# Kernel optimization log

Measured on AMD Instinct MI355X. Metric: run time of the kernel, lower is better.

## Reference

```python
import jax, jax.numpy as jnp
import numpy as np

B, T, D_IN, D_MODEL = 4, 4096, 256, 128


def setup_inputs() -> dict:
    key = jax.random.key(0)
    ks = jax.random.split(key, 7)
    s_in = 1.0 / np.sqrt(D_IN)
    return {
        "x": jax.random.normal(ks[0], (B, T, D_IN), dtype=jnp.float32),
        "Wq": jax.random.normal(ks[1], (D_IN, D_MODEL), dtype=jnp.float32) * s_in,
        "bq": jnp.zeros((D_MODEL,), dtype=jnp.float32),
        "Wk": jax.random.normal(ks[2], (D_IN, D_MODEL), dtype=jnp.float32) * s_in,
        "bk": jnp.zeros((D_MODEL,), dtype=jnp.float32),
        "Wv": jax.random.normal(ks[3], (D_IN, D_MODEL), dtype=jnp.float32) * s_in,
        "bv": jnp.zeros((D_MODEL,), dtype=jnp.float32),
    }


def reference(x, Wq, bq, Wk, bk, Wv, bv):
    # projections: (B,T,d_in) @ (d_in,d_model) -> (B,T,d_model)
    q = x @ Wq + bq
    k = x @ Wk + bk
    v = x @ Wv + bv
    # scores: (B,T,T), scaled by sqrt(d_model)
    scores = jnp.einsum("btd,bsd->bts", q, k) / np.sqrt(D_MODEL).astype(np.float32)
    attn = jax.nn.softmax(scores, axis=-1)
    out = jnp.einsum("bts,bsd->btd", attn, v)
    return out, attn
```

## Files before the change

### kernel.cpp

```cpp
#include <hip/hip_runtime.h>
#include <hip/hip_bf16.h>
#include <stdint.h>

#define TT 4096
#define DM 128
#define DIN 256
#define NB 4

typedef __attribute__((ext_vector_type(4))) float f32x4;
typedef __attribute__((ext_vector_type(8))) short s16x8;
typedef __attribute__((ext_vector_type(4))) short s16x4;
typedef __attribute__((ext_vector_type(4))) int i32x4;

union v4u { i32x4 u; s16x8 h; };

__device__ __forceinline__ unsigned short f2bf(float f) {
    union { float f; unsigned int u; } v; v.f = f;
    return (unsigned short)((v.u + 0x7FFFu + ((v.u >> 16) & 1u)) >> 16);
}

__device__ __forceinline__ void cp16(const void* g, void* l) {
    __builtin_amdgcn_global_load_lds(
        (__attribute__((address_space(1))) unsigned int*)(size_t)g,
        (__attribute__((address_space(3))) unsigned int*)l, 16, 0, 0);
}

__global__ __launch_bounds__(256) void k_wt(const float* __restrict__ Wq,
                                            const float* __restrict__ Wk,
                                            const float* __restrict__ Wv,
                                            unsigned short* __restrict__ Wtb) {
    int tid = blockIdx.x * 256 + threadIdx.x;
    int m = tid >> 15;
    int r = tid & 32767;
    int n = r >> 8;
    int k = r & 255;
    const float* W = (m == 0) ? Wq : (m == 1) ? Wk : Wv;
    Wtb[(size_t)tid] = f2bf(W[k * DM + n]);
}

__global__ __launch_bounds__(256) void k_proj(const float* __restrict__ x,
        const float* __restrict__ bq, const float* __restrict__ bk, const float* __restrict__ bv,
        const unsigned short* __restrict__ Wtb,
        unsigned short* __restrict__ Qb, unsigned short* __restrict__ Kb,
        unsigned short* __restrict__ Vb) {
    __shared__ __align__(16) unsigned short wt[DM][40];
    __shared__ __align__(16) unsigned short xl[64][40];
    int m = blockIdx.x >> 8;
    int tile = blockIdx.x & 255;
    int rowbase = tile * 64;
    int i = threadIdx.x;
    int w = i >> 6, l = i & 63;
    int lg = l >> 4, ll = l & 15;
    const float* bias = (m == 0) ? bq : (m == 1) ? bk : bv;
    unsigned short* out = (m == 0) ? Qb : (m == 1) ? Kb : Vb;
    const unsigned short* wsrc = Wtb + (size_t)m * DM * DIN;

    f32x4 acc[8];
    for (int n = 0; n < 8; n++) acc[n] = (f32x4){0.f, 0.f, 0.f, 0.f};

    for (int kk = 0; kk < 8; kk++) {
        int k0 = kk * 32;
        for (int t = 0; t < 2; t++) {
            int idx = i + t * 256;
            int row = idx >> 2, c8 = idx & 3;
            s16x8 v = *(const s16x8*)(wsrc + (size_t)row * DIN + k0 + c8 * 8);
            *(s16x8*)(&wt[row][c8 * 8]) = v;
        }
        for (int t = 0; t < 2; t++) {
            int idx = i + t * 256;
            int row = idx >> 3, c4 = idx & 7;
            f32x4 v = *(const f32x4*)(x + (size_t)(rowbase + row) * DIN + k0 + c4 * 4);
            s16x4 h;
            for (int j = 0; j < 4; j++) h[j] = (short)f2bf(v[j]);
            *(s16x4*)(&xl[row][c4 * 4]) = h;
        }
        __syncthreads();
        s16x8 a = *(const s16x8*)(&xl[w * 16 + ll][lg * 8]);
        for (int n = 0; n < 8; n++) {
            s16x8 b = *(const s16x8*)(&wt[n * 16 + ll][lg * 8]);
            acc[n] = __builtin_amdgcn_mfma_f32_16x16x32_bf16(a, b, acc[n], 0, 0, 0);
        }
        __syncthreads();
    }
    for (int n = 0; n < 8; n++) {
        int col = n * 16 + ll;
        float bv_ = bias[col];
        for (int j = 0; j < 4; j++) {
            int row = rowbase + w * 16 + lg * 4 + j;
            out[(size_t)row * DM + col] = f2bf(acc[n][j] + bv_);
        }
    }
}

__global__ __launch_bounds__(256) void k_vt(const unsigned short* __restrict__ Vb,
                                            unsigned short* __restrict__ Vtb) {
    __shared__ __align__(16) unsigned short tile[64][72];
    int bid = blockIdx.x;
    int b = bid >> 7;
    int rem = bid & 127;
    int tI = rem >> 1, dI = rem & 1;
    int t0 = tI * 64, d0 = dI * 64;
    int i = threadIdx.x;
    for (int t = 0; t < 2; t++) {
        int idx = i + t * 256;
        int r = idx >> 3, c8 = idx & 7;
        s16x8 v = *(const s16x8*)(Vb + ((size_t)(b * TT) + t0 + r) * DM + d0 + c8 * 8);
        *(s16x8*)(&tile[r][c8 * 8]) = v;
    }
    __syncthreads();
    for (int t = 0; t < 2; t++) {
        int idx = i + t * 256;
        int r2 = idx >> 3, c8 = idx & 7;
        s16x8 v;
        for (int j = 0; j < 8; j++) v[j] = (short)tile[c8 * 8 + j][r2];
        *(s16x8*)(Vtb + ((size_t)b * DM + d0 + r2) * TT + t0 + c8 * 8) = v;
    }
}

__global__ __launch_bounds__(512, 4) void k_attn(const unsigned short* __restrict__ Qb,
        const unsigned short* __restrict__ Kb, const unsigned short* __restrict__ Vtb,
        float* __restrict__ outO, float* __restrict__ outA) {
    __shared__ __align__(16) char smem[66048];

    int bid = blockIdx.x;
    int id2 = (bid & 7) * 64 + (bid >> 3);
    int b = id2 >> 7;
    int rowbase = (id2 & 127) * 32;
    int i = threadIdx.x;
    int w = i >> 6, l = i & 63;
    int rg = w & 1, ks = w >> 1;
    int lg = l >> 4, ll = l & 15;

    const unsigned short* Qrow = Qb + ((size_t)(b * TT) + rowbase) * DM;
    const unsigned short* Krow = Kb + (size_t)(b * TT) * DM;
    const unsigned short* Vt_b = Vtb + (size_t)b * DM * TT;
    const float scale = 0.08838834764831845f;

    float* rsx = (float*)(smem + 65536);

    s16x8 qf[4];
    for (int c = 0; c < 4; c++)
        qf[c] = *(const s16x8*)(Qrow + (size_t)(rg * 16 + ll) * DM + c * 32 + lg * 8);

    int kr = ks * 16 + ll;

    auto stage_k = [&](char* kbuf, int s0) {
        for (int u = 0; u < 2; u++) {
            int ch = u * 8 + w;
            int row = ch * 4 + (l >> 4);
            int g = (l & 15) ^ (row & 7);
            cp16(Krow + (size_t)(s0 + row) * DM + g * 8, kbuf + ch * 1024);
        }
    };
    auto stage_v = [&](char* vbuf, int s0) {
        for (int u = 0; u < 2; u++) {
            int ch = u * 8 + w;
            int row = ch * 8 + (l >> 3);
            int g = (l & 7) ^ (row & 7);
            cp16(Vt_b + (size_t)row * TT + s0 + g * 8, vbuf + ch * 1024);
        }
    };
    auto qk = [&](const char* kbuf) -> f32x4 {
        const char* kbase = kbuf + kr * 256;
        f32x4 acc = (f32x4){0.f, 0.f, 0.f, 0.f};
        for (int c = 0; c < 4; c++) {
            s16x8 kf = *(const s16x8*)(kbase + (((c * 4 + lg) ^ (kr & 7)) << 4));
            acc = __builtin_amdgcn_mfma_f32_16x16x32_bf16(kf, qf[c], acc, 0, 0, 0);
        }
        return acc;
    };

    float rs = 0.f;
    stage_k(smem, 0);
    stage_k(smem + 16384, 64);
    asm volatile("s_waitcnt vmcnt(2)" ::: "memory");
    __builtin_amdgcn_s_barrier();
    for (int t = 0; t < 64; t++) {
        if (t + 2 < 64) stage_k(smem + ((t + 2) & 3) * 16384, (t + 2) * 64);
        asm volatile("" ::: "memory");
        f32x4 acc = qk(smem + (t & 3) * 16384);
        for (int j = 0; j < 4; j++) rs += __expf(acc[j] * scale);
        if (t + 2 < 64) asm volatile("s_waitcnt vmcnt(2)" ::: "memory");
        else            asm volatile("s_waitcnt vmcnt(0)" ::: "memory");
        __builtin_amdgcn_s_barrier();
    }
    rs += __shfl_xor(rs, 16, 64);
    rs += __shfl_xor(rs, 32, 64);
    if (lg == 0) rsx[w * 16 + ll] = rs;
    __syncthreads();
    float inv = 1.0f / (rsx[(0 * 2 + rg) * 16 + ll] + rsx[(1 * 2 + rg) * 16 + ll]
                      + rsx[(2 * 2 + rg) * 16 + ll] + rsx[(3 * 2 + rg) * 16 + ll]);

    f32x4 oacc[8];
    for (int n = 0; n < 8; n++) oacc[n] = (f32x4){0.f, 0.f, 0.f, 0.f};

    float* Arow = outA + ((size_t)(b * TT) + rowbase + rg * 16 + ll) * TT + ks * 16 + lg * 4;
    int a0addr = (((2 * lg) & 3) * 16 + ll) * 4;
    int a1addr = (((2 * lg + 1) & 3) * 16 + ll) * 4;
    int gi = ks * 2 + (lg & 1);

    stage_k(smem, 0);
    stage_v(smem + 32768, 0);
    asm volatile("s_waitcnt vmcnt(0)" ::: "memory");
    __builtin_amdgcn_s_barrier();

    for (int t = 0; t < 64; t++) {
        size_t s0 = (size_t)t * 64;
        if (t < 63) {
            stage_k(smem + ((t + 1) & 1) * 16384, t * 64 + 64);
            stage_v(smem + 32768 + ((t + 1) & 1) * 16384, t * 64 + 64);
        }
        asm volatile("" ::: "memory");
        f32x4 acc = qk(smem + (t & 1) * 16384);
        f32x4 p;
        for (int j = 0; j < 4; j++) p[j] = __expf(acc[j] * scale) * inv;
        __builtin_nontemporal_store(p, (f32x4*)(Arow + s0));
        unsigned u0 = (unsigned)f2bf(p[0]) | ((unsigned)f2bf(p[1]) << 16);
        unsigned u1 = (unsigned)f2bf(p[2]) | ((unsigned)f2bf(p[3]) << 16);
        int b0 = __builtin_amdgcn_ds_bpermute(a0addr, (int)u0);
        int b1 = __builtin_amdgcn_ds_bpermute(a0addr, (int)u1);
        int b2 = __builtin_amdgcn_ds_bpermute(a1addr, (int)u0);
        int b3 = __builtin_amdgcn_ds_bpermute(a1addr, (int)u1);
        v4u pa;
        pa.u = (lg < 2) ? (i32x4){b0, b1, b2, b3} : (i32x4){0, 0, 0, 0};
        const char* vbuf = smem + 32768 + (t & 1) * 16384;
        for (int n = 0; n < 8; n++) {
            int vr = n * 16 + ll;
            s16x8 bfr = *(const s16x8*)(vbuf + vr * 128 + ((gi ^ (vr & 7)) << 4));
            oacc[n] = __builtin_amdgcn_mfma_f32_16x16x32_bf16(pa.h, bfr, oacc[n], 0, 0, 0);
        }
        asm volatile("s_waitcnt vmcnt(1)" ::: "memory");
        __builtin_amdgcn_s_barrier();
    }

    float* obuf = (float*)smem;
    if (ks > 0) {
        float* dst = obuf + (size_t)(rg * 3 + ks - 1) * 16 * 132;
        for (int n = 0; n < 8; n++)
            for (int j = 0; j < 4; j++)
                dst[(lg * 4 + j) * 132 + n * 16 + ll] = oacc[n][j];
    }
    __syncthreads();
    if (ks == 0) {
        float* d0 = obuf + (size_t)(rg * 3 + 0) * 16 * 132;
        float* d1 = obuf + (size_t)(rg * 3 + 1) * 16 * 132;
        float* d2 = obuf + (size_t)(rg * 3 + 2) * 16 * 132;
        for (int n = 0; n < 8; n++)
            for (int j = 0; j < 4; j++) {
                int idx = (lg * 4 + j) * 132 + n * 16 + ll;
                d0[idx] = oacc[n][j] + d0[idx] + d1[idx] + d2[idx];
            }
    }
    __syncthreads();
    {
        int row = i >> 4;
        int col = (i & 15) * 8;
        const float* src = obuf + (size_t)((row >> 4) * 3) * 16 * 132 + (row & 15) * 132 + col;
        f32x4 v0 = *(const f32x4*)(src);
        f32x4 v1 = *(const f32x4*)(src + 4);
        float* dst = outO + ((size_t)(b * TT) + rowbase + row) * DM + col;
        *(f32x4*)dst = v0;
        *(f32x4*)(dst + 4) = v1;
    }
}

extern "C" void kernel_launch(void* const* d_in, const int* in_sizes, int n_in,
                              void* d_out, int out_size, void* d_ws, size_t ws_size,
                              hipStream_t stream) {
    const float* x  = (const float*)d_in[0];
    const float* Wq = (const float*)d_in[1];
    const float* bq = (const float*)d_in[2];
    const float* Wk = (const float*)d_in[3];
    const float* bk = (const float*)d_in[4];
    const float* Wv = (const float*)d_in[5];
    const float* bv = (const float*)d_in[6];
    float* outO = (float*)d_out;
    float* outA = outO + (size_t)NB * TT * DM;

    char* ws = (char*)d_ws;
    unsigned short* Qb  = (unsigned short*)(ws);
    unsigned short* Kb  = (unsigned short*)(ws + ((size_t)1 << 22));
    unsigned short* Vb  = (unsigned short*)(ws + ((size_t)2 << 22));
    unsigned short* Vtb = (unsigned short*)(ws + ((size_t)3 << 22));
    unsigned short* Wtb = (unsigned short*)(ws + ((size_t)4 << 22));

    k_wt<<<dim3(384), dim3(256), 0, stream>>>(Wq, Wk, Wv, Wtb);
    k_proj<<<dim3(768), dim3(256), 0, stream>>>(x, bq, bk, bv, Wtb, Qb, Kb, Vb);
    k_vt<<<dim3(512), dim3(256), 0, stream>>>(Vb, Vtb);
    k_attn<<<dim3(512), dim3(512), 0, stream>>>(Qb, Kb, Vtb, outO, outA);
}
```

Before: 145.3 us.

## Warp-specialize second attention pass into producer QK waves and consumer PV waves

The second pass is split by wave. Four waves compute QK^T and the softmax probabilities for 32-column tiles and write fp32 and bf16 P tiles into shared memory. The other four waves stream V, run the PV MFMAs one tile behind, and write the attention matrix out from shared memory. Each consumer wave owns a distinct output slice, so the cross-wave reduction of O through shared memory is no longer needed. The change uses more LDS, which may reduce occupancy, and the tile-sized steps double the number of barriers.

```diff
diff --git a/kernel.cpp b/kernel.cpp
--- a/kernel.cpp
+++ b/kernel.cpp
@@ -10,9 +10,7 @@
 typedef __attribute__((ext_vector_type(4))) float f32x4;
 typedef __attribute__((ext_vector_type(8))) short s16x8;
 typedef __attribute__((ext_vector_type(4))) short s16x4;
-typedef __attribute__((ext_vector_type(4))) int i32x4;
-
-union v4u { i32x4 u; s16x8 h; };
+typedef __attribute__((ext_vector_type(2))) unsigned int u32x2;
 
 __device__ __forceinline__ unsigned short f2bf(float f) {
     union { float f; unsigned int u; } v; v.f = f;
@@ -120,7 +118,7 @@
 __global__ __launch_bounds__(512, 4) void k_attn(const unsigned short* __restrict__ Qb,
         const unsigned short* __restrict__ Kb, const unsigned short* __restrict__ Vtb,
         float* __restrict__ outO, float* __restrict__ outA) {
-    __shared__ __align__(16) char smem[66048];
+    __shared__ __align__(16) char smem[79360];
 
     int bid = blockIdx.x;
     int id2 = (bid & 7) * 64 + (bid >> 3);
@@ -128,139 +126,175 @@
     int rowbase = (id2 & 127) * 32;
     int i = threadIdx.x;
     int w = i >> 6, l = i & 63;
-    int rg = w & 1, ks = w >> 1;
     int lg = l >> 4, ll = l & 15;
+    int rh = w & 1;
 
     const unsigned short* Qrow = Qb + ((size_t)(b * TT) + rowbase) * DM;
     const unsigned short* Krow = Kb + (size_t)(b * TT) * DM;
     const unsigned short* Vt_b = Vtb + (size_t)b * DM * TT;
     const float scale = 0.08838834764831845f;
 
-    float* rsx = (float*)(smem + 65536);
+    float* rsx = (float*)(smem + 78848);
 
     s16x8 qf[4];
     for (int c = 0; c < 4; c++)
-        qf[c] = *(const s16x8*)(Qrow + (size_t)(rg * 16 + ll) * DM + c * 32 + lg * 8);
-
-    int kr = ks * 16 + ll;
-
-    auto stage_k = [&](char* kbuf, int s0) {
-        for (int u = 0; u < 2; u++) {
-            int ch = u * 8 + w;
-            int row = ch * 4 + (l >> 4);
-            int g = (l & 15) ^ (row & 7);
-            cp16(Krow + (size_t)(s0 + row) * DM + g * 8, kbuf + ch * 1024);
-        }
-    };
-    auto stage_v = [&](char* vbuf, int s0) {
-        for (int u = 0; u < 2; u++) {
-            int ch = u * 8 + w;
-            int row = ch * 8 + (l >> 3);
-            int g = (l & 7) ^ (row & 7);
-            cp16(Vt_b + (size_t)row * TT + s0 + g * 8, vbuf + ch * 1024);
-        }
-    };
-    auto qk = [&](const char* kbuf) -> f32x4 {
-        const char* kbase = kbuf + kr * 256;
-        f32x4 acc = (f32x4){0.f, 0.f, 0.f, 0.f};
-        for (int c = 0; c < 4; c++) {
-            s16x8 kf = *(const s16x8*)(kbase + (((c * 4 + lg) ^ (kr & 7)) << 4));
-            acc = __builtin_amdgcn_mfma_f32_16x16x32_bf16(kf, qf[c], acc, 0, 0, 0);
-        }
-        return acc;
-    };
+        qf[c] = *(const s16x8*)(Qrow + (size_t)(rh * 16 + ll) * DM + c * 32 + lg * 8);
 
     float rs = 0.f;
-    stage_k(smem, 0);
-    stage_k(smem + 16384, 64);
-    asm volatile("s_waitcnt vmcnt(2)" ::: "memory");
-    __builtin_amdgcn_s_barrier();
-    for (int t = 0; t < 64; t++) {
-        if (t + 2 < 64) stage_k(smem + ((t + 2) & 3) * 16384, (t + 2) * 64);
-        asm volatile("" ::: "memory");
-        f32x4 acc = qk(smem + (t & 3) * 16384);
-        for (int j = 0; j < 4; j++) rs += __expf(acc[j] * scale);
-        if (t + 2 < 64) asm volatile("s_waitcnt vmcnt(2)" ::: "memory");
-        else            asm volatile("s_waitcnt vmcnt(0)" ::: "memory");
+    {
+        int ks = w >> 1;
+        int kr = ks * 16 + ll;
+        auto stage1 = [&](int slot, int t) {
+            int s0 = t * 64;
+            for (int u = 0; u < 2; u++) {
+                int c = u * 8 + w;
+                int row = c * 4 + (l >> 4);
+                int g = (l & 15) ^ (row & 7);
+                cp16(Krow + (size_t)(s0 + row) * DM + g * 8, smem + slot * 16384 + c * 1024);
+            }
+        };
+        stage1(0, 0); stage1(1, 1);
+        asm volatile("s_waitcnt vmcnt(2)" ::: "memory");
         __builtin_amdgcn_s_barrier();
+        int cur = 0, nxt = 2;
+        for (int t = 0; t < 64; t++) {
+            if (t + 2 < 64) stage1(nxt, t + 2);
+            const char* kbase = smem + cur * 16384 + kr * 256;
+            f32x4 acc = (f32x4){0.f, 0.f, 0.f, 0.f};
+            for (int c = 0; c < 4; c++) {
+                s16x8 kf = *(const s16x8*)(kbase + (((c * 4 + lg) ^ (kr & 7)) << 4));
+                acc = __builtin_amdgcn_mfma_f32_16x16x32_bf16(kf, qf[c], acc, 0, 0, 0);
+            }
+            for (int j = 0; j < 4; j++) rs += __expf(acc[j] * scale);
+            if (t + 2 < 64) asm volatile("s_waitcnt vmcnt(2)" ::: "memory");
+            else            asm volatile("s_waitcnt vmcnt(0)" ::: "memory");
+            __builtin_amdgcn_s_barrier();
+            cur++; if (cur == 3) cur = 0;
+            nxt++; if (nxt == 3) nxt = 0;
+        }
     }
     rs += __shfl_xor(rs, 16, 64);
     rs += __shfl_xor(rs, 32, 64);
-    if (lg == 0) rsx[w * 16 + ll] = rs;
+    if (l < 16) rsx[w * 16 + l] = rs;
     __syncthreads();
-    float inv = 1.0f / (rsx[(0 * 2 + rg) * 16 + ll] + rsx[(1 * 2 + rg) * 16 + ll]
-                      + rsx[(2 * 2 + rg) * 16 + ll] + rsx[(3 * 2 + rg) * 16 + ll]);
-
-    f32x4 oacc[8];
-    for (int n = 0; n < 8; n++) oacc[n] = (f32x4){0.f, 0.f, 0.f, 0.f};
-
-    float* Arow = outA + ((size_t)(b * TT) + rowbase + rg * 16 + ll) * TT + ks * 16 + lg * 4;
-    int a0addr = (((2 * lg) & 3) * 16 + ll) * 4;
-    int a1addr = (((2 * lg + 1) & 3) * 16 + ll) * 4;
-    int gi = ks * 2 + (lg & 1);
-
-    stage_k(smem, 0);
-    stage_v(smem + 32768, 0);
-    asm volatile("s_waitcnt vmcnt(0)" ::: "memory");
-    __builtin_amdgcn_s_barrier();
-
-    for (int t = 0; t < 64; t++) {
-        size_t s0 = (size_t)t * 64;
-        if (t < 63) {
-            stage_k(smem + ((t + 1) & 1) * 16384, t * 64 + 64);
-            stage_v(smem + 32768 + ((t + 1) & 1) * 16384, t * 64 + 64);
-        }
-        asm volatile("" ::: "memory");
-        f32x4 acc = qk(smem + (t & 1) * 16384);
-        f32x4 p;
-        for (int j = 0; j < 4; j++) p[j] = __expf(acc[j] * scale) * inv;
-        __builtin_nontemporal_store(p, (f32x4*)(Arow + s0));
-        unsigned u0 = (unsigned)f2bf(p[0]) | ((unsigned)f2bf(p[1]) << 16);
-        unsigned u1 = (unsigned)f2bf(p[2]) | ((unsigned)f2bf(p[3]) << 16);
-        int b0 = __builtin_amdgcn_ds_bpermute(a0addr, (int)u0);
-        int b1 = __builtin_amdgcn_ds_bpermute(a0addr, (int)u1);
-        int b2 = __builtin_amdgcn_ds_bpermute(a1addr, (int)u0);
-        int b3 = __builtin_amdgcn_ds_bpermute(a1addr, (int)u1);
-        v4u pa;
-        pa.u = (lg < 2) ? (i32x4){b0, b1, b2, b3} : (i32x4){0, 0, 0, 0};
-        const char* vbuf = smem + 32768 + (t & 1) * 16384;
-        for (int n = 0; n < 8; n++) {
-            int vr = n * 16 + ll;
-            s16x8 bfr = *(const s16x8*)(vbuf + vr * 128 + ((gi ^ (vr & 7)) << 4));
-            oacc[n] = __builtin_amdgcn_mfma_f32_16x16x32_bf16(pa.h, bfr, oacc[n], 0, 0, 0);
-        }
-        asm volatile("s_waitcnt vmcnt(1)" ::: "memory");
-        __builtin_amdgcn_s_barrier();
-    }
-
-    float* obuf = (float*)smem;
-    if (ks > 0) {
-        float* dst = obuf + (size_t)(rg * 3 + ks - 1) * 16 * 132;
-        for (int n = 0; n < 8; n++)
-            for (int j = 0; j < 4; j++)
-                dst[(lg * 4 + j) * 132 + n * 16 + ll] = oacc[n][j];
-    }
+    float inv = 0.f;
+    if (w < 4)
+        inv = 1.0f / (rsx[rh * 16 + ll] + rsx[(2 + rh) * 16 + ll]
+                    + rsx[(4 + rh) * 16 + ll] + rsx[(6 + rh) * 16 + ll]);
+
+    char* kslotb = smem;
+    char* vslotb = smem + 24576;
+    float* PfB = (float*)(smem + 57344);
+    unsigned short* PbB = (unsigned short*)(smem + 71168);
+
+    f32x4 oacc[4];
+    for (int n = 0; n < 4; n++) oacc[n] = (f32x4){0.f, 0.f, 0.f, 0.f};
+
+    int kh = w >> 1;
+    int kr2 = kh * 16 + ll;
+    int cw = w - 4;
+    int r2 = cw & 1, c2 = cw >> 1;
+
+    auto stageK = [&](int slot, int t) {
+        int s0 = t * 32;
+        for (int u = 0; u < 2; u++) {
+            int c = u * 4 + w;
+            int row = c * 4 + (l >> 4);
+            int g = (l & 15) ^ (row & 7);
+            cp16(Krow + (size_t)(s0 + row) * DM + g * 8, kslotb + slot * 8192 + c * 1024);
+        }
+    };
+    auto stageV = [&](int slot, int t) {
+        int s0 = t * 32;
+        for (int u = 0; u < 2; u++) {
+            int c = u * 4 + cw;
+            int row = c * 16 + (l >> 2);
+            int g = (l & 3) ^ (row & 3);
+            cp16(Vt_b + (size_t)row * TT + s0 + g * 8, vslotb + slot * 8192 + c * 1024);
+        }
+    };
+
+    if (w < 4) { stageK(0, 0); stageK(1, 1);
+                 asm volatile("s_waitcnt vmcnt(2)" ::: "memory"); }
+    else       { stageV(0, 0); stageV(1, 1); }
     __syncthreads();
-    if (ks == 0) {
-        float* d0 = obuf + (size_t)(rg * 3 + 0) * 16 * 132;
-        float* d1 = obuf + (size_t)(rg * 3 + 1) * 16 * 132;
-        float* d2 = obuf + (size_t)(rg * 3 + 2) * 16 * 132;
-        for (int n = 0; n < 8; n++)
+
+    int pk_cur = 0, pk_nxt = 2;
+    int cP = 2, cV = 3, cVn = 2;
+
+    for (int t = 0; t < 128; t++) {
+        if (w < 4) {
+            if (t + 2 <= 127) stageK(pk_nxt, t + 2);
+            const char* kbase = kslotb + pk_cur * 8192 + kr2 * 256;
+            f32x4 acc = (f32x4){0.f, 0.f, 0.f, 0.f};
+            for (int c = 0; c < 4; c++) {
+                s16x8 kf = *(const s16x8*)(kbase + (((c * 4 + lg) ^ (kr2 & 7)) << 4));
+                acc = __builtin_amdgcn_mfma_f32_16x16x32_bf16(kf, qf[c], acc, 0, 0, 0);
+            }
+            f32x4 p;
+            for (int j = 0; j < 4; j++) p[j] = __expf(acc[j] * scale) * inv;
+            int prow = rh * 16 + ll;
+            *(f32x4*)(PfB + pk_cur * 1152 + prow * 36 + kh * 16 + lg * 4) = p;
+            u32x2 pb;
+            pb[0] = (unsigned)f2bf(p[0]) | ((unsigned)f2bf(p[1]) << 16);
+            pb[1] = (unsigned)f2bf(p[2]) | ((unsigned)f2bf(p[3]) << 16);
+            *(u32x2*)(PbB + pk_cur * 1280 + prow * 40 + kh * 16 + lg * 4) = pb;
+            asm volatile("s_waitcnt lgkmcnt(0)" ::: "memory");
+            if (t < 126) asm volatile("s_waitcnt vmcnt(2)" ::: "memory");
+            else         asm volatile("s_waitcnt vmcnt(0)" ::: "memory");
+            __builtin_amdgcn_s_barrier();
+            pk_cur++; if (pk_cur == 3) pk_cur = 0;
+            pk_nxt++; if (pk_nxt == 3) pk_nxt = 0;
+        } else {
+            __builtin_amdgcn_s_barrier();
+            if (t + 2 <= 127) stageV(cVn, t + 2);
+            if (t < 2)        asm volatile("s_waitcnt vmcnt(4)" ::: "memory");
+            else if (t < 126) asm volatile("s_waitcnt vmcnt(5)" ::: "memory");
+            else if (t == 126) asm volatile("s_waitcnt vmcnt(3)" ::: "memory");
+            else              asm volatile("s_waitcnt vmcnt(1)" ::: "memory");
+            if (t >= 1) {
+                s16x8 pa = *(const s16x8*)(PbB + cP * 1280 + (r2 * 16 + ll) * 40 + lg * 8);
+                const char* vb = vslotb + cV * 8192;
+                for (int n8 = 0; n8 < 4; n8++) {
+                    int vr = c2 * 64 + n8 * 16 + ll;
+                    s16x8 bf = *(const s16x8*)(vb + vr * 64 + ((lg ^ (vr & 3)) << 4));
+                    oacc[n8] = __builtin_amdgcn_mfma_f32_16x16x32_bf16(pa, bf, oacc[n8], 0, 0, 0);
+                }
+                int arow = cw * 8 + (l >> 3);
+                int acol = (l & 7) * 4;
+                f32x4 av = *(const f32x4*)(PfB + cP * 1152 + arow * 36 + acol);
+                __builtin_nontemporal_store(av,
+                    (f32x4*)(outA + ((size_t)(b * TT) + rowbase + arow) * TT
+                             + (size_t)(t - 1) * 32 + acol));
+            }
+            cP++; if (cP == 3) cP = 0;
+            cV++; if (cV == 4) cV = 0;
+            cVn++; if (cVn == 4) cVn = 0;
+        }
+    }
+
+    if (w >= 4) {
+        s16x8 pa = *(const s16x8*)(PbB + 1 * 1280 + (r2 * 16 + ll) * 40 + lg * 8);
+        const char* vb = vslotb + 3 * 8192;
+        for (int n8 = 0; n8 < 4; n8++) {
+            int vr = c2 * 64 + n8 * 16 + ll;
+            s16x8 bf = *(const s16x8*)(vb + vr * 64 + ((lg ^ (vr & 3)) << 4));
+            oacc[n8] = __builtin_amdgcn_mfma_f32_16x16x32_bf16(pa, bf, oacc[n8], 0, 0, 0);
+        }
+        {
+            int arow = cw * 8 + (l >> 3);
+            int acol = (l & 7) * 4;
+            f32x4 av = *(const f32x4*)(PfB + 1 * 1152 + arow * 36 + acol);
+            __builtin_nontemporal_store(av,
+                (f32x4*)(outA + ((size_t)(b * TT) + rowbase + arow) * TT
+                         + (size_t)127 * 32 + acol));
+        }
+        for (int n8 = 0; n8 < 4; n8++)
             for (int j = 0; j < 4; j++) {
-                int idx = (lg * 4 + j) * 132 + n * 16 + ll;
-                d0[idx] = oacc[n][j] + d0[idx] + d1[idx] + d2[idx];
-            }
-    }
-    __syncthreads();
-    {
-        int row = i >> 4;
-        int col = (i & 15) * 8;
-        const float* src = obuf + (size_t)((row >> 4) * 3) * 16 * 132 + (row & 15) * 132 + col;
-        f32x4 v0 = *(const f32x4*)(src);
-        f32x4 v1 = *(const f32x4*)(src + 4);
-        float* dst = outO + ((size_t)(b * TT) + rowbase + row) * DM + col;
-        *(f32x4*)dst = v0;
-        *(f32x4*)(dst + 4) = v1;
+                int row = r2 * 16 + lg * 4 + j;
+                int col = c2 * 64 + n8 * 16 + ll;
+                outO[((size_t)(b * TT) + rowbase + row) * DM + col] = oacc[n8][j];
+            }
     }
 }
 
```

Result: faster. 137.2 us (-5.6%).
